# Kernel optimization log

Measured on AMD Instinct MI355X. Metric: run time of the kernel, lower is better.

## Reference

```python
import jax, jax.numpy as jnp
from jax import lax
import numpy as np

N_SEQ, BATCH, HID = 512, 32, 1024

def setup_inputs() -> dict:
    key = jax.random.key(0)
    k1, k2, k3 = jax.random.split(key, 3)
    Y = jax.random.normal(k1, (N_SEQ, BATCH, 3 * HID), dtype=jnp.float32)
    init_c = jax.random.normal(k2, (1, BATCH, HID), dtype=jnp.float32)
    init_h = jax.random.normal(k3, (1, BATCH, HID), dtype=jnp.float32)
    return {"Y": Y, "init_c": init_c, "init_h": init_h}

def reference(Y, init_c, init_h):
    # QRNN fo-pooling: c_t = f_t * c_{t-1} + (1 - f_t) * z_t ; h_t = o_t * c_t
    # Zoneout dropout is evaluated in inference mode (identity), so F is used as-is.
    F, Z, O = jnp.split(Y, 3, axis=2)       # each [T, B, H]
    F = jax.nn.sigmoid(F)
    Z = jnp.tanh(Z)
    O = jax.nn.sigmoid(O)
    ZF = (1.0 - F) * Z

    def step(c, inp):
        f, zf, o = inp
        c = f * c + zf
        return c, c * o

    _, h = lax.scan(step, init_c[0], (F, ZF, O))  # h: [T, B, H]
    return jnp.concatenate([init_h, h], axis=0)   # [T+1, B, H]
```

## Files before the change

kernel.cpp:

```cpp
#include <hip/hip_runtime.h>


#define T_SEQ 512
#define BATCH 32
#define HID   1024
#define CH    (BATCH * HID)
#define CH4   (CH / 4)
#define HID4  (HID / 4)
#define ROWS4 (BATCH * 3 * HID4)
#define NC    64
#define CL    (T_SEQ / NC)
#define JW    16
#define NTHR  (NC * JW)

__device__ __forceinline__ float fast_sigmoid(float x) {
    float e = __builtin_amdgcn_exp2f(-1.4426950408889634f * x);
    return __builtin_amdgcn_rcpf(1.0f + e);
}
__device__ __forceinline__ float fast_tanh(float x) {
    float e = __builtin_amdgcn_exp2f(-2.8853900817779268f * x);
    float s = __builtin_amdgcn_rcpf(1.0f + e);
    return __builtin_fmaf(2.0f, s, -1.0f);
}
__device__ __forceinline__ float4 sig4(float4 v) {
    return make_float4(fast_sigmoid(v.x), fast_sigmoid(v.y),
                       fast_sigmoid(v.z), fast_sigmoid(v.w));
}
__device__ __forceinline__ float4 tanh4(float4 v) {
    return make_float4(fast_tanh(v.x), fast_tanh(v.y),
                       fast_tanh(v.z), fast_tanh(v.w));
}

__global__ __launch_bounds__(NTHR, 4) void fo_pool_fused(
        const float4* __restrict__ Y4,
        const float4* __restrict__ init_c4,
        const float4* __restrict__ init_h4,
        float4* __restrict__ out4) {
    __shared__ float4 sA[NC][JW];
    __shared__ float4 sB[NC][JW];

    const int tid = threadIdx.x;
    const int k   = tid >> 4;
    const int j   = tid & (JW - 1);
    const int c4  = blockIdx.x * JW + j;
    const int b   = c4 >> 8;
    const int h4  = c4 & (HID4 - 1);
    const float4* yb = Y4 + b * (3 * HID4) + h4 + (size_t)(k * CL) * ROWS4;

    float4 ff[CL], gg[CL];
    float4 A = make_float4(1.f, 1.f, 1.f, 1.f);
    float4 B = make_float4(0.f, 0.f, 0.f, 0.f);

    float4 f0 = yb[0], z0 = yb[HID4];
#pragma unroll
    for (int t = 0; t < CL; ++t) {
        float4 f1, z1;
        if (t + 1 < CL) {
            const float4* p = yb + (size_t)(t + 1) * ROWS4;
            f1 = p[0]; z1 = p[HID4];
        }
        float4 s  = sig4(f0);
        float4 th = tanh4(z0);
        float4 g  = make_float4((1.f - s.x) * th.x, (1.f - s.y) * th.y,
                                (1.f - s.z) * th.z, (1.f - s.w) * th.w);
        ff[t] = s; gg[t] = g;
        B.x = __builtin_fmaf(s.x, B.x, g.x);
        B.y = __builtin_fmaf(s.y, B.y, g.y);
        B.z = __builtin_fmaf(s.z, B.z, g.z);
        B.w = __builtin_fmaf(s.w, B.w, g.w);
        A.x *= s.x; A.y *= s.y; A.z *= s.z; A.w *= s.w;
        f0 = f1; z0 = z1;
    }
    sA[k][j] = A;
    sB[k][j] = B;
    __syncthreads();

    if (tid < JW) {
        const int cc4 = blockIdx.x * JW + tid;
        out4[cc4] = init_h4[cc4];
        float4 c = init_c4[cc4];
#pragma unroll
        for (int kk = 0; kk < NC; ++kk) {
            float4 a  = sA[kk][tid];
            float4 b0 = sB[kk][tid];
            sA[kk][tid] = c;
            c.x = __builtin_fmaf(a.x, c.x, b0.x);
            c.y = __builtin_fmaf(a.y, c.y, b0.y);
            c.z = __builtin_fmaf(a.z, c.z, b0.z);
            c.w = __builtin_fmaf(a.w, c.w, b0.w);
        }
    }
    __syncthreads();

    float4 c = sA[k][j];
    float4* ob = out4 + (size_t)(k * CL + 1) * CH4 + c4;

    float4 o0 = yb[2 * HID4];
#pragma unroll
    for (int t = 0; t < CL; ++t) {
        float4 o1;
        if (t + 1 < CL) o1 = (yb + (size_t)(t + 1) * ROWS4)[2 * HID4];
        c.x = __builtin_fmaf(ff[t].x, c.x, gg[t].x);
        c.y = __builtin_fmaf(ff[t].y, c.y, gg[t].y);
        c.z = __builtin_fmaf(ff[t].z, c.z, gg[t].z);
        c.w = __builtin_fmaf(ff[t].w, c.w, gg[t].w);
        float4 oo = sig4(o0);
        float4 hh = make_float4(c.x * oo.x, c.y * oo.y, c.z * oo.z, c.w * oo.w);
        ob[(size_t)t * CH4] = hh;
        o0 = o1;
    }
}

extern "C" void kernel_launch(void* const* d_in, const int* in_sizes, int n_in,
                              void* d_out, int out_size, void* d_ws, size_t ws_size,
                              hipStream_t stream) {
    const float* Y      = (const float*)d_in[0];
    const float* init_c = (const float*)d_in[1];
    const float* init_h = (const float*)d_in[2];
    float* out = (float*)d_out;

    fo_pool_fused<<<CH4 / JW, NTHR, 0, stream>>>(
        (const float4*)Y, (const float4*)init_c, (const float4*)init_h, (float4*)out);
}
```

Measured before the change: 306.6 us.

## Replace serial chunk combine with Hillis-Steele scan and shorten chunks

Doubles the number of time chunks per block (CL drops from 8 to 4) and halves the channel width per block. The single-thread serial combine across chunks is replaced by a parallel log-step Hillis-Steele scan over the (A,B) pairs in shared memory, with init_c applied afterwards. All F/Z loads and all O loads for a chunk are now issued up front to raise memory-level parallelism. In exchange the kernel adds many __syncthreads rounds, and the occupancy hint in the launch bounds is dropped.

```diff
diff --git a/kernel.cpp b/kernel.cpp
--- a/kernel.cpp
+++ b/kernel.cpp
@@ -8,9 +8,9 @@
 #define CH4   (CH / 4)
 #define HID4  (HID / 4)
 #define ROWS4 (BATCH * 3 * HID4)
-#define NC    64
+#define NC    128
 #define CL    (T_SEQ / NC)
-#define JW    16
+#define JW    8
 #define NTHR  (NC * JW)
 
 __device__ __forceinline__ float fast_sigmoid(float x) {
@@ -26,12 +26,12 @@
     return make_float4(fast_sigmoid(v.x), fast_sigmoid(v.y),
                        fast_sigmoid(v.z), fast_sigmoid(v.w));
 }
-__device__ __forceinline__ float4 tanh4(float4 v) {
-    return make_float4(fast_tanh(v.x), fast_tanh(v.y),
-                       fast_tanh(v.z), fast_tanh(v.w));
+__device__ __forceinline__ float4 fma4(float4 a, float4 b, float4 c) {
+    return make_float4(__builtin_fmaf(a.x, b.x, c.x), __builtin_fmaf(a.y, b.y, c.y),
+                       __builtin_fmaf(a.z, b.z, c.z), __builtin_fmaf(a.w, b.w, c.w));
 }
 
-__global__ __launch_bounds__(NTHR, 4) void fo_pool_fused(
+__global__ __launch_bounds__(NTHR) void fo_pool_fused(
         const float4* __restrict__ Y4,
         const float4* __restrict__ init_c4,
         const float4* __restrict__ init_h4,
@@ -40,74 +40,72 @@
     __shared__ float4 sB[NC][JW];
 
     const int tid = threadIdx.x;
-    const int k   = tid >> 4;
+    const int k   = tid >> 3;
     const int j   = tid & (JW - 1);
     const int c4  = blockIdx.x * JW + j;
     const int b   = c4 >> 8;
     const int h4  = c4 & (HID4 - 1);
     const float4* yb = Y4 + b * (3 * HID4) + h4 + (size_t)(k * CL) * ROWS4;
 
-    float4 ff[CL], gg[CL];
-    float4 A = make_float4(1.f, 1.f, 1.f, 1.f);
-    float4 B = make_float4(0.f, 0.f, 0.f, 0.f);
-
-    float4 f0 = yb[0], z0 = yb[HID4];
+    float4 fr[CL], zr[CL];
 #pragma unroll
     for (int t = 0; t < CL; ++t) {
-        float4 f1, z1;
-        if (t + 1 < CL) {
-            const float4* p = yb + (size_t)(t + 1) * ROWS4;
-            f1 = p[0]; z1 = p[HID4];
-        }
-        float4 s  = sig4(f0);
-        float4 th = tanh4(z0);
-        float4 g  = make_float4((1.f - s.x) * th.x, (1.f - s.y) * th.y,
-                                (1.f - s.z) * th.z, (1.f - s.w) * th.w);
+        const float4* p = yb + (size_t)t * ROWS4;
+        fr[t] = p[0]; zr[t] = p[HID4];
+    }
+    float4 ff[CL], gg[CL];
+    float4 A  = make_float4(1.f, 1.f, 1.f, 1.f);
+    float4 Bv = make_float4(0.f, 0.f, 0.f, 0.f);
+#pragma unroll
+    for (int t = 0; t < CL; ++t) {
+        float4 s = sig4(fr[t]);
+        float4 g;
+        g.x = (1.f - s.x) * fast_tanh(zr[t].x);
+        g.y = (1.f - s.y) * fast_tanh(zr[t].y);
+        g.z = (1.f - s.z) * fast_tanh(zr[t].z);
+        g.w = (1.f - s.w) * fast_tanh(zr[t].w);
         ff[t] = s; gg[t] = g;
-        B.x = __builtin_fmaf(s.x, B.x, g.x);
-        B.y = __builtin_fmaf(s.y, B.y, g.y);
-        B.z = __builtin_fmaf(s.z, B.z, g.z);
-        B.w = __builtin_fmaf(s.w, B.w, g.w);
+        Bv = fma4(s, Bv, g);
         A.x *= s.x; A.y *= s.y; A.z *= s.z; A.w *= s.w;
-        f0 = f1; z0 = z1;
     }
     sA[k][j] = A;
-    sB[k][j] = B;
+    sB[k][j] = Bv;
     __syncthreads();
 
-    if (tid < JW) {
-        const int cc4 = blockIdx.x * JW + tid;
-        out4[cc4] = init_h4[cc4];
-        float4 c = init_c4[cc4];
 #pragma unroll
-        for (int kk = 0; kk < NC; ++kk) {
-            float4 a  = sA[kk][tid];
-            float4 b0 = sB[kk][tid];
-            sA[kk][tid] = c;
-            c.x = __builtin_fmaf(a.x, c.x, b0.x);
-            c.y = __builtin_fmaf(a.y, c.y, b0.y);
-            c.z = __builtin_fmaf(a.z, c.z, b0.z);
-            c.w = __builtin_fmaf(a.w, c.w, b0.w);
+    for (int d = 1; d < NC; d <<= 1) {
+        float4 pa, pb;
+        const bool has = (k >= d);
+        if (has) { pa = sA[k - d][j]; pb = sB[k - d][j]; }
+        __syncthreads();
+        if (has) {
+            float4 a  = sA[k][j];
+            float4 bb = sB[k][j];
+            sA[k][j] = make_float4(a.x * pa.x, a.y * pa.y, a.z * pa.z, a.w * pa.w);
+            sB[k][j] = fma4(a, pb, bb);
         }
+        __syncthreads();
     }
-    __syncthreads();
 
-    float4 c = sA[k][j];
+    const float4 c0 = init_c4[c4];
+    float4 c;
+    if (k == 0) {
+        c = c0;
+        out4[c4] = init_h4[c4];
+    } else {
+        c = fma4(sA[k - 1][j], c0, sB[k - 1][j]);
+    }
+
+    float4 orr[CL];
+#pragma unroll
+    for (int t = 0; t < CL; ++t) orr[t] = (yb + (size_t)t * ROWS4)[2 * HID4];
+
     float4* ob = out4 + (size_t)(k * CL + 1) * CH4 + c4;
-
-    float4 o0 = yb[2 * HID4];
 #pragma unroll
     for (int t = 0; t < CL; ++t) {
-        float4 o1;
-        if (t + 1 < CL) o1 = (yb + (size_t)(t + 1) * ROWS4)[2 * HID4];
-        c.x = __builtin_fmaf(ff[t].x, c.x, gg[t].x);
-        c.y = __builtin_fmaf(ff[t].y, c.y, gg[t].y);
-        c.z = __builtin_fmaf(ff[t].z, c.z, gg[t].z);
-        c.w = __builtin_fmaf(ff[t].w, c.w, gg[t].w);
-        float4 oo = sig4(o0);
-        float4 hh = make_float4(c.x * oo.x, c.y * oo.y, c.z * oo.z, c.w * oo.w);
-        ob[(size_t)t * CH4] = hh;
-        o0 = o1;
+        c = fma4(ff[t], c, gg[t]);
+        float4 oo = sig4(orr[t]);
+        ob[(size_t)t * CH4] = make_float4(c.x * oo.x, c.y * oo.y, c.z * oo.z, c.w * oo.w);
     }
 }
 
```

New measurement: 312.0 us. Within noise of the previous version (+1.7%).
